# Optimization experiments

Measured on AMD Instinct MI355X. Metric: run time of the kernel, lower is better.

The kernel has to match this reference:

```python
import jax, jax.numpy as jnp
import numpy as np

D_MODEL = 256
B = 4
Q_PER_IMAGE = 256
FEATS_PER_IMAGE = 65536
HW = 512


def setup_inputs() -> dict:
    key = jax.random.key(0)
    ks = jax.random.split(key, 12)
    queries = jax.random.normal(ks[0], (B * Q_PER_IMAGE, D_MODEL), dtype=jnp.float32)
    feature_values = jax.random.normal(ks[1], (B * FEATS_PER_IMAGE, D_MODEL), dtype=jnp.float32)
    # sparse COO indices of the full-scale feature map: (batch, h, w), batch-sorted
    batch_col = jnp.repeat(jnp.arange(B, dtype=jnp.int64), FEATS_PER_IMAGE)
    hw = jax.random.randint(ks[2], (B * FEATS_PER_IMAGE, 2), 0, HW).astype(jnp.int64)
    feature_indices = jnp.concatenate([batch_col[:, None], hw], axis=-1)
    query_batch_offsets = (jnp.arange(B, dtype=jnp.int64) * Q_PER_IMAGE)
    # MLP params: torch nn.Linear convention y = x @ W.T + b, W: [out, in]
    scale = 1.0 / np.sqrt(D_MODEL)
    params = {}
    for i in range(4):
        params[f"W{i+1}"] = jax.random.uniform(ks[3 + 2 * i], (D_MODEL, D_MODEL), jnp.float32, -scale, scale)
        params[f"b{i+1}"] = jax.random.uniform(ks[4 + 2 * i], (D_MODEL,), jnp.float32, -scale, scale)
    return {
        "queries": queries,
        "feature_values": feature_values,
        "feature_indices": feature_indices,
        "query_batch_offsets": query_batch_offsets,
        **params,
    }


def reference(queries, feature_values, feature_indices, query_batch_offsets,
              W1, b1, W2, b2, W3, b3, W4, b4):
    x = queries
    for W, b in ((W1, b1), (W2, b2), (W3, b3)):
        x = jax.nn.relu(x @ W.T + b)
    x = x @ W4.T + b4  # [B*Q, d]

    nb = query_batch_offsets.shape[0]
    d = x.shape[-1]
    q = x.reshape(nb, -1, d)                    # [B, Q, d] per-image query splits
    feats = feature_values.reshape(nb, -1, d)   # [B, Nf, d] per-image feature splits
    # per-image torch.mm(im_feats, im_queries.T), batched
    logits = jnp.einsum("bnd,bqd->bnq", feats, q)  # values of the output sparse COO tensor
    # Output sparse indices are (feature_indices[i], q) for each local query q;
    # the values (in index order) are exactly `logits`.
    return logits
```

## Files before the change

### kernel.cpp

```cpp
#include <hip/hip_runtime.h>
#include <hip/hip_bf16.h>

#define D_MODEL 256
#define N_ROWS  262144
#define N_Q     1024

typedef __attribute__((ext_vector_type(8))) short short8;
typedef __attribute__((ext_vector_type(16))) float floatx16;

static __device__ __forceinline__ short f2bf(float x) {
    union { __hip_bfloat16 h; short s; } u;
    u.h = __float2bfloat16(x);
    return u.s;
}

__global__ __launch_bounds__(256) void mlp_kernel(
    const float* __restrict__ q,
    const float* __restrict__ W1, const float* __restrict__ b1,
    const float* __restrict__ W2, const float* __restrict__ b2,
    const float* __restrict__ W3, const float* __restrict__ b3,
    const float* __restrict__ W4, const float* __restrict__ b4,
    __hip_bfloat16* __restrict__ xout)
{
    __shared__ float cur[4][D_MODEL];
    const int j = threadIdx.x;
    const int row0 = blockIdx.x * 4;

    #pragma unroll
    for (int i = 0; i < 4; i++)
        cur[i][j] = q[(long)(row0 + i) * D_MODEL + j];
    __syncthreads();

    const float* Ws[4] = { W1, W2, W3, W4 };
    const float* bs[4] = { b1, b2, b3, b4 };

    for (int l = 0; l < 4; l++) {
        const float4* wrow = (const float4*)(Ws[l] + (long)j * D_MODEL);
        float acc0 = bs[l][j];
        float acc1 = acc0, acc2 = acc0, acc3 = acc0;
        #pragma unroll 8
        for (int k = 0; k < D_MODEL / 4; k++) {
            float4 w  = wrow[k];
            float4 c0 = ((const float4*)cur[0])[k];
            float4 c1 = ((const float4*)cur[1])[k];
            float4 c2 = ((const float4*)cur[2])[k];
            float4 c3 = ((const float4*)cur[3])[k];
            acc0 += w.x*c0.x + w.y*c0.y + w.z*c0.z + w.w*c0.w;
            acc1 += w.x*c1.x + w.y*c1.y + w.z*c1.z + w.w*c1.w;
            acc2 += w.x*c2.x + w.y*c2.y + w.z*c2.z + w.w*c2.w;
            acc3 += w.x*c3.x + w.y*c3.y + w.z*c3.z + w.w*c3.w;
        }
        __syncthreads();
        if (l < 3) {
            cur[0][j] = fmaxf(acc0, 0.f);
            cur[1][j] = fmaxf(acc1, 0.f);
            cur[2][j] = fmaxf(acc2, 0.f);
            cur[3][j] = fmaxf(acc3, 0.f);
            __syncthreads();
        } else {
            xout[(long)(row0 + 0) * D_MODEL + j] = __float2bfloat16(acc0);
            xout[(long)(row0 + 1) * D_MODEL + j] = __float2bfloat16(acc1);
            xout[(long)(row0 + 2) * D_MODEL + j] = __float2bfloat16(acc2);
            xout[(long)(row0 + 3) * D_MODEL + j] = __float2bfloat16(acc3);
        }
    }
}

#define APAD 264
#define BM   32
#define TILES_PER_BLOCK 8

__global__ __launch_bounds__(256) void logits_kernel(
    const float* __restrict__ F,
    const __hip_bfloat16* __restrict__ X,
    float* __restrict__ out)
{
    __shared__ __hip_bfloat16 As[BM * APAD];

    const int t    = threadIdx.x;
    const int wave = t >> 6;
    const int lane = t & 63;
    const int m    = lane & 31;
    const int kg   = lane >> 5;

    int b = blockIdx.x;
    b = (b & 7) * (1024 / 8) + (b >> 3);

    const long row00 = (long)b * (BM * TILES_PER_BLOCK);
    const int  batch = (int)(row00 >> 16);

    const __hip_bfloat16* bb =
        X + ((long)(batch << 8) + (wave << 6) + m) * D_MODEL + kg * 8;

    float4 pend[8];
    {
        const float4* Fb = (const float4*)(F + row00 * D_MODEL);
        #pragma unroll
        for (int i = 0; i < 8; i++)
            pend[i] = Fb[i * 256 + t];
    }

    for (int tt = 0; tt < TILES_PER_BLOCK; tt++) {
        #pragma unroll
        for (int i = 0; i < 8; i++) {
            const int flat = i * 256 + t;
            const int row  = flat >> 6;
            const int c4   = (flat & 63) << 2;
            union { ushort4 u; short s[4]; } w;
            w.s[0] = f2bf(pend[i].x); w.s[1] = f2bf(pend[i].y);
            w.s[2] = f2bf(pend[i].z); w.s[3] = f2bf(pend[i].w);
            *(ushort4*)(&As[row * APAD + c4]) = w.u;
        }
        __syncthreads();

        if (tt < TILES_PER_BLOCK - 1) {
            const float4* Fb =
                (const float4*)(F + (row00 + (long)(tt + 1) * BM) * D_MODEL);
            #pragma unroll
            for (int i = 0; i < 8; i++)
                pend[i] = Fb[i * 256 + t];
        }

        const __hip_bfloat16* a0 = &As[m * APAD + kg * 8];
        floatx16 acc0 = {0.f}, acc1 = {0.f};

        #pragma unroll 4
        for (int ks = 0; ks < 16; ks++) {
            const int k0 = ks * 16;
            short8 af  = *(const short8*)(a0 + k0);
            short8 bf0 = *(const short8*)(bb + k0);
            short8 bf1 = *(const short8*)(bb + 32 * D_MODEL + k0);
            acc0 = __builtin_amdgcn_mfma_f32_32x32x16_bf16(af, bf0, acc0, 0, 0, 0);
            acc1 = __builtin_amdgcn_mfma_f32_32x32x16_bf16(af, bf1, acc1, 0, 0, 0);
        }

        const long rbase   = row00 + (long)tt * BM + 4 * kg;
        const int  colbase = (wave << 6) + m;
        #pragma unroll
        for (int reg = 0; reg < 16; reg++) {
            const int r = (reg & 3) + 8 * (reg >> 2);
            float* orow = out + (rbase + r) * D_MODEL + colbase;
            __builtin_nontemporal_store(acc0[reg], orow);
            __builtin_nontemporal_store(acc1[reg], orow + 32);
        }

        __syncthreads();
    }
}

extern "C" void kernel_launch(void* const* d_in, const int* in_sizes, int n_in,
                              void* d_out, int out_size, void* d_ws, size_t ws_size,
                              hipStream_t stream) {
    const float* queries = (const float*)d_in[0];
    const float* feats   = (const float*)d_in[1];
    const float* W1 = (const float*)d_in[4];
    const float* b1 = (const float*)d_in[5];
    const float* W2 = (const float*)d_in[6];
    const float* b2 = (const float*)d_in[7];
    const float* W3 = (const float*)d_in[8];
    const float* b3 = (const float*)d_in[9];
    const float* W4 = (const float*)d_in[10];
    const float* b4 = (const float*)d_in[11];

    __hip_bfloat16* x_bf16 = (__hip_bfloat16*)d_ws;

    mlp_kernel<<<N_Q / 4, 256, 0, stream>>>(queries, W1, b1, W2, b2, W3, b3, W4, b4, x_bf16);
    logits_kernel<<<N_ROWS / (BM * TILES_PER_BLOCK), 256, 0, stream>>>(
        feats, x_bf16, (float*)d_out);
}
```

Baseline: 612.8 us.

## Process one 32-row tile per block and drop register prefetch pipeline

```diff
diff --git a/kernel.cpp b/kernel.cpp
--- a/kernel.cpp
+++ b/kernel.cpp
@@ -68,9 +68,8 @@
 
 #define APAD 264
 #define BM   32
-#define TILES_PER_BLOCK 8
 
-__global__ __launch_bounds__(256) void logits_kernel(
+__global__ __launch_bounds__(256, 6) void logits_kernel(
     const float* __restrict__ F,
     const __hip_bfloat16* __restrict__ X,
     float* __restrict__ out)
@@ -84,67 +83,51 @@
     const int kg   = lane >> 5;
 
     int b = blockIdx.x;
-    b = (b & 7) * (1024 / 8) + (b >> 3);
+    b = (b & 7) * (8192 / 8) + (b >> 3);
 
-    const long row00 = (long)b * (BM * TILES_PER_BLOCK);
-    const int  batch = (int)(row00 >> 16);
+    const long row0  = (long)b * BM;
+    const int  batch = (int)(row0 >> 16);
 
-    const __hip_bfloat16* bb =
-        X + ((long)(batch << 8) + (wave << 6) + m) * D_MODEL + kg * 8;
-
-    float4 pend[8];
     {
-        const float4* Fb = (const float4*)(F + row00 * D_MODEL);
-        #pragma unroll
-        for (int i = 0; i < 8; i++)
-            pend[i] = Fb[i * 256 + t];
-    }
-
-    for (int tt = 0; tt < TILES_PER_BLOCK; tt++) {
+        const float4* Fb = (const float4*)(F + row0 * D_MODEL);
         #pragma unroll
         for (int i = 0; i < 8; i++) {
             const int flat = i * 256 + t;
             const int row  = flat >> 6;
             const int c4   = (flat & 63) << 2;
+            float4 v = Fb[flat];
             union { ushort4 u; short s[4]; } w;
-            w.s[0] = f2bf(pend[i].x); w.s[1] = f2bf(pend[i].y);
-            w.s[2] = f2bf(pend[i].z); w.s[3] = f2bf(pend[i].w);
+            w.s[0] = f2bf(v.x); w.s[1] = f2bf(v.y);
+            w.s[2] = f2bf(v.z); w.s[3] = f2bf(v.w);
             *(ushort4*)(&As[row * APAD + c4]) = w.u;
         }
-        __syncthreads();
+    }
+    __syncthreads();
 
-        if (tt < TILES_PER_BLOCK - 1) {
-            const float4* Fb =
-                (const float4*)(F + (row00 + (long)(tt + 1) * BM) * D_MODEL);
-            #pragma unroll
-            for (int i = 0; i < 8; i++)
-                pend[i] = Fb[i * 256 + t];
-        }
+    const __hip_bfloat16* a0 = &As[m * APAD + kg * 8];
+    const __hip_bfloat16* bb =
+        X + ((long)(batch << 8) + (wave << 6) + m) * D_MODEL + kg * 8;
 
-        const __hip_bfloat16* a0 = &As[m * APAD + kg * 8];
-        floatx16 acc0 = {0.f}, acc1 = {0.f};
+    floatx16 acc0 = {0.f}, acc1 = {0.f};
 
-        #pragma unroll 4
-        for (int ks = 0; ks < 16; ks++) {
-            const int k0 = ks * 16;
-            short8 af  = *(const short8*)(a0 + k0);
-            short8 bf0 = *(const short8*)(bb + k0);
-            short8 bf1 = *(const short8*)(bb + 32 * D_MODEL + k0);
-            acc0 = __builtin_amdgcn_mfma_f32_32x32x16_bf16(af, bf0, acc0, 0, 0, 0);
-            acc1 = __builtin_amdgcn_mfma_f32_32x32x16_bf16(af, bf1, acc1, 0, 0, 0);
-        }
+    #pragma unroll 4
+    for (int ks = 0; ks < 16; ks++) {
+        const int k0 = ks * 16;
+        short8 af  = *(const short8*)(a0 + k0);
+        short8 bf0 = *(const short8*)(bb + k0);
+        short8 bf1 = *(const short8*)(bb + 32 * D_MODEL + k0);
+        acc0 = __builtin_amdgcn_mfma_f32_32x32x16_bf16(af, bf0, acc0, 0, 0, 0);
+        acc1 = __builtin_amdgcn_mfma_f32_32x32x16_bf16(af, bf1, acc1, 0, 0, 0);
+    }
 
-        const long rbase   = row00 + (long)tt * BM + 4 * kg;
-        const int  colbase = (wave << 6) + m;
-        #pragma unroll
-        for (int reg = 0; reg < 16; reg++) {
-            const int r = (reg & 3) + 8 * (reg >> 2);
-            float* orow = out + (rbase + r) * D_MODEL + colbase;
-            __builtin_nontemporal_store(acc0[reg], orow);
-            __builtin_nontemporal_store(acc1[reg], orow + 32);
-        }
-
-        __syncthreads();
+    const long rbase   = row0 + 4 * kg;
+    const int  colbase = (wave << 6) + m;
+    #pragma unroll
+    for (int reg = 0; reg < 16; reg++) {
+        const int r = (reg & 3) + 8 * (reg >> 2);
+        float* orow = out + (rbase + r) * D_MODEL + colbase;
+        __builtin_nontemporal_store(acc0[reg], orow);
+        __builtin_nontemporal_store(acc1[reg], orow + 32);
     }
 }
 
@@ -165,6 +148,5 @@
     __hip_bfloat16* x_bf16 = (__hip_bfloat16*)d_ws;
 
     mlp_kernel<<<N_Q / 4, 256, 0, stream>>>(queries, W1, b1, W2, b2, W3, b3, W4, b4, x_bf16);
-    logits_kernel<<<N_ROWS / (BM * TILES_PER_BLOCK), 256, 0, stream>>>(
-        feats, x_bf16, (float*)d_out);
+    logits_kernel<<<N_ROWS / BM, 256, 0, stream>>>(feats, x_bf16, (float*)d_out);
 }
```

New measurement: 620.2 us. No clear change (+1.2%).
